# Kernel optimization log

Hardware: AMD Instinct MI355X
Metric: run time of the kernel (lower is better)

Reference implementation:

```python
import jax, jax.numpy as jnp
import numpy as np


def _conv(x, w, b):
    # x: [N,Cin,H,W], w: [Cout,Cin,kh,kw]
    y = jax.lax.conv_general_dilated(x, w, (1, 1), 'SAME',
                                     dimension_numbers=('NCHW', 'OIHW', 'NCHW'))
    return y + b[None, :, None, None]


def _up2(x):
    n, c, h, w = x.shape
    return jax.image.resize(x, (n, c, 2 * h, 2 * w), method='bilinear')


def setup_inputs() -> dict:
    key = jax.random.key(0)
    ks = jax.random.split(key, 24)
    N, C, H, W = 4, 256, 128, 128
    D, L, NUM_CLASSES = 512, 8, 75
    f32 = jnp.float32

    def rn(k, shape, scale=0.02):
        return jax.random.normal(k, shape, dtype=f32) * scale

    inp = {
        'p2': jax.random.normal(ks[0], (N, C, H, W), dtype=f32),
        'p3': jax.random.normal(ks[1], (N, C, H // 2, W // 2), dtype=f32),
        'p4': jax.random.normal(ks[2], (N, C, H // 4, W // 4), dtype=f32),
        'p5': jax.random.normal(ks[3], (N, C, H // 8, W // 8), dtype=f32),
        'rel_coord': jax.random.normal(ks[4], (N, 2, H, W), dtype=f32),
        'abs_coord': jax.random.normal(ks[5], (N, 2, H, W), dtype=f32),
        'fg_mask': jax.random.randint(ks[6], (N, 1, H, W), 0, 2, dtype=jnp.int32),
    }
    # scale-head convs: p2 x1 (no up), p3 x1 (+up), p4 x2 (+up each), p5 x3 (+up each)
    for i, nm in enumerate(['w_p2_0', 'w_p3_0', 'w_p4_0', 'w_p4_1', 'w_p5_0', 'w_p5_1', 'w_p5_2']):
        inp[nm] = rn(ks[7 + i], (C, C, 3, 3))
        inp['b' + nm[1:]] = jnp.zeros((C,), f32)
    # comb_pe_conv: (conv_dims + pe_dim) -> conv_dims, 3x3
    inp['comb_w'] = rn(ks[14], (C, C + 4, 3, 3))
    inp['comb_b'] = jnp.zeros((C,), f32)
    # densepose sparse head: 8 stacked submanifold 3x3 convs, dim 512
    inp['head_w0'] = rn(ks[15], (D, C, 3, 3))
    inp['head_b0'] = jnp.zeros((D,), f32)
    inp['head_w'] = rn(ks[16], (L - 1, D, D, 3, 3))
    inp['head_b'] = jnp.zeros((L - 1, D), f32)
    # predictor: 1x1 conv to num_classes
    inp['pred_w'] = rn(ks[17], (NUM_CLASSES, D, 1, 1))
    inp['pred_b'] = jnp.zeros((NUM_CLASSES,), f32)
    return inp


def reference(p2, p3, p4, p5, rel_coord, abs_coord, fg_mask,
              w_p2_0, b_p2_0, w_p3_0, b_p3_0, w_p4_0, b_p4_0, w_p4_1, b_p4_1,
              w_p5_0, b_p5_0, w_p5_1, b_p5_1, w_p5_2, b_p5_2,
              comb_w, comb_b, head_w0, head_b0, head_w, head_b, pred_w, pred_b):
    relu = jax.nn.relu
    # FPN scale heads merged to common stride
    x = relu(_conv(p2, w_p2_0, b_p2_0))
    x = x + _up2(relu(_conv(p3, w_p3_0, b_p3_0)))
    t = _up2(relu(_conv(p4, w_p4_0, b_p4_0)))
    x = x + _up2(relu(_conv(t, w_p4_1, b_p4_1)))
    t = _up2(relu(_conv(p5, w_p5_0, b_p5_0)))
    t = _up2(relu(_conv(t, w_p5_1, b_p5_1)))
    x = x + _up2(relu(_conv(t, w_p5_2, b_p5_2)))
    # concat positional encodings, comb conv
    x = jnp.concatenate([x, rel_coord, abs_coord], axis=1)  # [N, C+4, H, W]
    x = relu(_conv(x, comb_w, comb_b))
    # sparse gather -> submanifold sparse conv head -> dense scatter.
    # Masking inputs and outputs at each layer is math-equivalent to spconv's
    # SparseConvTensor built from fg_mask-active coords, SubM convs, then .dense().
    mask = (fg_mask > 0).astype(x.dtype)  # [N,1,H,W]
    h = x * mask
    h = relu(_conv(h, head_w0, head_b0)) * mask
    for i in range(head_w.shape[0]):
        h = relu(_conv(h, head_w[i], head_b[i])) * mask
    # dense predictor (1x1 conv) on scattered dense tensor
    return _conv(h, pred_w, pred_b)  # [N, 75, H, W]
```

## Files before the change

kernel.cpp:

```cpp
#include <hip/hip_runtime.h>
#include <cstdint>
#include <cstddef>

#define THREADS 256

typedef _Float16 f16x8 __attribute__((ext_vector_type(8)));
typedef _Float16 f16x4 __attribute__((ext_vector_type(4)));
typedef _Float16 f16x2 __attribute__((ext_vector_type(2)));
typedef float f32x4 __attribute__((ext_vector_type(4)));
typedef float f32x8 __attribute__((ext_vector_type(8)));

__device__ __forceinline__ void gll16(const void* g, void* l) {
    __builtin_amdgcn_global_load_lds(
        (const __attribute__((address_space(1))) unsigned int*)g,
        (__attribute__((address_space(3))) unsigned int*)l, 16, 0, 0);
}

__global__ void pack_scale_all_kernel(
    const float* __restrict__ w0, const float* __restrict__ w1,
    const float* __restrict__ w2, const float* __restrict__ w3,
    const float* __restrict__ w4, const float* __restrict__ w5,
    const float* __restrict__ w6, const float* __restrict__ w7,
    _Float16* __restrict__ wp)
{
    const int wi = blockIdx.y;
    const float* w = (wi == 0) ? w0 : (wi == 1) ? w1 : (wi == 2) ? w2 : (wi == 3) ? w3
                   : (wi == 4) ? w4 : (wi == 5) ? w5 : (wi == 6) ? w6 : w7;
    const int Cin = (wi == 7) ? 260 : 256;
    const int CC  = (wi == 7) ? 9 : 8;
    _Float16* dst = wp + (size_t)wi * 663552;
    int idx = blockIdx.x * THREADS + threadIdx.x;
    int total = 256 * CC * 4;
    if (idx >= total) return;
    int u = idx & 3;
    int cc = (idx >> 2) % CC;
    int co = (idx >> 2) / CC;
    int ci0 = cc * 32 + u * 8;
    for (int tap = 0; tap < 9; ++tap) {
        f16x8 v;
#pragma unroll
        for (int j = 0; j < 8; ++j) {
            int ci = ci0 + j;
            v[j] = (ci < Cin) ? (_Float16)w[((size_t)co * Cin + ci) * 9 + tap] : (_Float16)0.f;
        }
        *reinterpret_cast<f16x8*>(dst + ((((size_t)tap * CC + cc) * 4 + u) * 256 + co) * 8) = v;
    }
}

__global__ void pack_wdense_kernel(const float* __restrict__ w, _Float16* __restrict__ wp,
                                   int CinTrue, int CINP)
{
    const int NSTEP = 9 * (CINP / 64);
    int idx = blockIdx.x * THREADS + threadIdx.x;
    if (idx >= 256 * NSTEP * 8) return;
    int kc = idx & 7;
    int t = (idx >> 3) % NSTEP;
    int co = (idx >> 3) / NSTEP;
    int kcs = kc ^ (co & 7);
    int k = t * 64 + kcs * 8;
    int tap = k / CINP;
    int cib = k - tap * CINP;
    f16x8 v;
#pragma unroll
    for (int j = 0; j < 8; ++j) {
        int ci = cib + j;
        v[j] = (ci < CinTrue) ? (_Float16)w[((size_t)co * CinTrue + ci) * 9 + tap] : (_Float16)0.f;
    }
    *reinterpret_cast<f16x8*>(wp + ((size_t)t * 2048 + co * 8 + kc) * 8) = v;
}

__global__ void pack_whead_all_kernel(const float* __restrict__ hw0,
                                      const float* __restrict__ hw,
                                      _Float16* __restrict__ wp0,
                                      _Float16* __restrict__ wpH)
{
    const int wi = blockIdx.y;
    const int Cin = (wi == 0) ? 256 : 512;
    const float* w = (wi == 0) ? hw0 : hw + (size_t)(wi - 1) * 2359296;
    _Float16* wp = (wi == 0) ? wp0 : wpH + (size_t)(wi - 1) * 2359296;
    const int NSTEP = 9 * (Cin / 64);
    int idx = blockIdx.x * THREADS + threadIdx.x;
    int total = 512 * NSTEP * 8;
    if (idx >= total) return;
    int kc = idx & 7;
    int t = (idx >> 3) % NSTEP;
    int co = (idx >> 3) / NSTEP;
    int gy = co >> 8;
    int r = co & 255;
    int kcs = kc ^ (r & 7);
    int k = t * 64 + kcs * 8;
    int tap = k / Cin;
    int cib = k - tap * Cin;
    f16x8 v;
#pragma unroll
    for (int j = 0; j < 8; ++j)
        v[j] = (_Float16)w[((size_t)co * Cin + cib + j) * 9 + tap];
    *reinterpret_cast<f16x8*>(wp + ((size_t)(t * 2 + gy) * 2048 + r * 8 + kc) * 8) = v;
}

__global__ void zerows_kernel(float* __restrict__ p)
{
    p[blockIdx.x * THREADS + threadIdx.x] = 0.f;
}

__global__ void zero2_kernel(_Float16* __restrict__ a, _Float16* __restrict__ b)
{
    const size_t N = 4ull * 16384 * 512;
    for (size_t i = ((size_t)blockIdx.x * THREADS + threadIdx.x) * 8; i < N;
         i += (size_t)gridDim.x * THREADS * 8) {
        *reinterpret_cast<f16x8*>(a + i) = (f16x8){};
        *reinterpret_cast<f16x8*>(b + i) = (f16x8){};
    }
}

__global__ __launch_bounds__(1024)
void compact_kernel(const int* __restrict__ fg, int* __restrict__ list)
{
    __shared__ int part[1024];
    const int tid = threadIdx.x;
    const int base = tid * 64;
    int cnt = 0;
    for (int j = 0; j < 64; ++j) cnt += (fg[base + j] > 0) ? 1 : 0;
    part[tid] = cnt;
    __syncthreads();
    for (int off = 1; off < 1024; off <<= 1) {
        int v = (tid >= off) ? part[tid - off] : 0;
        __syncthreads();
        part[tid] += v;
        __syncthreads();
    }
    int pos = part[tid] - cnt;
    for (int j = 0; j < 64; ++j)
        if (fg[base + j] > 0) list[pos++] = base + j;
    const int total = part[1023];
    for (int i = total + tid; i < 40960; i += 1024) list[i] = -1;
}

__global__ __launch_bounds__(256)
void t_all_kernel(const float* __restrict__ s2, const float* __restrict__ s3,
                  const float* __restrict__ s4, const float* __restrict__ s5,
                  _Float16* __restrict__ d2, _Float16* __restrict__ d3,
                  _Float16* __restrict__ d4, _Float16* __restrict__ d5)
{
    __shared__ _Float16 tile[64 * 32];
    const int lvl = blockIdx.z >> 2;
    const int n = blockIdx.z & 3;
    const int HW = 16384 >> (2 * lvl);
    const int p0 = blockIdx.x * 64;
    if (p0 >= HW) return;
    const float* in = (lvl == 0) ? s2 : (lvl == 1) ? s3 : (lvl == 2) ? s4 : s5;
    _Float16* out = (lvl == 0) ? d2 : (lvl == 1) ? d3 : (lvl == 2) ? d4 : d5;
    const int C = 256;
    const int c0 = blockIdx.y * 32;
    const int tid = threadIdx.x;
    {
        int ci = tid >> 3;
        int j8 = (tid & 7) * 8;
        f32x8 v = *reinterpret_cast<const f32x8*>(in + ((size_t)n * C + c0 + ci) * HW + p0 + j8);
#pragma unroll
        for (int j = 0; j < 8; ++j)
            tile[(j8 + j) * 32 + ci] = (_Float16)v[j];
    }
    __syncthreads();
    {
        int px = tid >> 2;
        int u = tid & 3;
        f16x8 v = *reinterpret_cast<const f16x8*>(&tile[px * 32 + u * 8]);
        *reinterpret_cast<f16x8*>(out + ((size_t)n * HW + p0 + px) * C + c0 + u * 8) = v;
    }
}

template<int INF32, int OUTMODE, int CC>
__global__ __launch_bounds__(512, 4)
void convu_kernel(const void* __restrict__ inv, const _Float16* __restrict__ wp,
                  const float* __restrict__ bias, const int* __restrict__ msk,
                  void* __restrict__ outp, int Cout, int H, int W,
                  int inCst, int outCst, int useMask)
{
    __shared__ _Float16 Xs[2 * 1344 * 8];

    const int tid = threadIdx.x;
    const int lane = tid & 63;
    const int wave = tid >> 6;
    const int lm = lane & 15;
    const int lu = lane >> 4;
    const int waveco = (wave & 1) * 64;
    const int wrow = (wave >> 1) * 4;
    const int n = blockIdx.z;
    const int co0 = blockIdx.y * 128;
    const int tpr = W >> 4;
    const int tx = blockIdx.x % tpr;
    const int ty = blockIdx.x / tpr;
    const int x0 = tx << 4;
    const int y0 = ty << 4;
    const int HW = H * W;

    int soff[3];
#pragma unroll
    for (int t = 0; t < 3; ++t) {
        int s = tid + t * 512;
        int item = s >> 2, u = s & 3;
        int row = item / 18, col = item - row * 18;
        int y = y0 + row - 1, x = x0 + col - 1;
        soff[t] = (s < 1296 && y >= 0 && y < H && x >= 0 && x < W)
                      ? ((n * HW + y * W + x) * inCst + u * 8) : -1;
    }

    f32x4 acc[4][4];
#pragma unroll
    for (int m = 0; m < 4; ++m)
#pragma unroll
        for (int nf = 0; nf < 4; ++nf)
            acc[m][nf] = (f32x4){0.f, 0.f, 0.f, 0.f};

    const size_t tstride = (size_t)CC * 4 * Cout * 8;

    {
        const _Float16* src = (const _Float16*)inv;
#pragma unroll
        for (int t = 0; t < 3; ++t) {
            int s = tid + t * 512;
            if (s < 1296 && soff[t] < 0) {
                *reinterpret_cast<f16x8*>(&Xs[s * 8]) = (f16x8){};
                *reinterpret_cast<f16x8*>(&Xs[(1344 + s) * 8]) = (f16x8){};
            }
        }
#pragma unroll
        for (int t = 0; t < 3; ++t) {
            int s = tid + t * 512;
            if (s < 1296 && soff[t] >= 0)
                gll16(src + soff[t], &Xs[(t * 512 + (tid & ~63)) * 8]);
        }
    }
    __syncthreads();

    int bsel = 0;
    for (int cc = 0; cc < CC; ++cc) {
        if (cc + 1 < CC) {
            const _Float16* src = (const _Float16*)inv;
#pragma unroll
            for (int t = 0; t < 3; ++t) {
                int s = tid + t * 512;
                if (s < 1296 && soff[t] >= 0)
                    gll16(src + soff[t] + (cc + 1) * 32,
                          &Xs[((bsel ^ 1) * 1344 + t * 512 + (tid & ~63)) * 8]);
            }
        }
        {
            const int xbase = bsel * 1344;
            const _Float16* wb = wp + (((size_t)cc * 4 + lu) * Cout + co0 + waveco + lm) * 8;
#pragma unroll
            for (int tap = 0; tap < 9; ++tap) {
                const int dy = tap / 3, dx = tap % 3;
                const _Float16* wt = wb + (size_t)tap * tstride;
                f16x8 a[4], b[4];
#pragma unroll
                for (int m = 0; m < 4; ++m)
                    a[m] = *reinterpret_cast<const f16x8*>(wt + m * 128);
#pragma unroll
                for (int nf = 0; nf < 4; ++nf) {
                    int slot = ((wrow + nf + dy) * 18 + lm + dx) * 4 + lu;
                    b[nf] = *reinterpret_cast<const f16x8*>(&Xs[(xbase + slot) * 8]);
                }
#pragma unroll
                for (int m = 0; m < 4; ++m)
#pragma unroll
                    for (int nf = 0; nf < 4; ++nf)
                        acc[m][nf] = __builtin_amdgcn_mfma_f32_16x16x32_f16(a[m], b[nf], acc[m][nf], 0, 0, 0);
            }
        }
        __syncthreads();
        bsel ^= 1;
    }

    const int xE = x0 + lm;
    const size_t nHW = (size_t)n * HW;
#pragma unroll
    for (int nf = 0; nf < 4; ++nf) {
        const int y = y0 + wrow + nf;
        float mv = 1.f;
        if (useMask) mv = (msk[nHW + y * W + xE] > 0) ? 1.f : 0.f;
        const size_t pixo = (nHW + (size_t)y * W + xE) * outCst;
#pragma unroll
        for (int m = 0; m < 4; ++m) {
            const int cb = co0 + waveco + m * 16 + lu * 4;
            const f32x4 bv = *reinterpret_cast<const f32x4*>(bias + cb);
            if (OUTMODE == 0) {
                f16x4 h;
#pragma unroll
                for (int r = 0; r < 4; ++r)
                    h[r] = (_Float16)(fmaxf(acc[m][nf][r] + bv[r], 0.f) * mv);
                *reinterpret_cast<f16x4*>((_Float16*)outp + pixo + cb) = h;
            } else if (OUTMODE == 1) {
                f32x4 v;
#pragma unroll
                for (int r = 0; r < 4; ++r)
                    v[r] = fmaxf(acc[m][nf][r] + bv[r], 0.f);
                *reinterpret_cast<f32x4*>((float*)outp + pixo + cb) = v;
            } else {
                f32x4 old = *reinterpret_cast<const f32x4*>((float*)outp + pixo + cb);
#pragma unroll
                for (int r = 0; r < 4; ++r)
                    old[r] += fmaxf(acc[m][nf][r] + bv[r], 0.f);
                *reinterpret_cast<f32x4*>((float*)outp + pixo + cb) = old;
            }
        }
    }
}

template<int CINP, int MASK>
__global__ __launch_bounds__(512, 1)
void gemm_dense_kernel(const _Float16* __restrict__ in,
                       const _Float16* __restrict__ wpk,
                       const float* __restrict__ bias,
                       const int* __restrict__ fg,
                       _Float16* __restrict__ outp, int outCst,
                       const _Float16* __restrict__ zpage)
{
    constexpr int SPT = CINP / 64;
    __shared__ __attribute__((aligned(16))) char ldsb[2 * 65536];

    const int job = blockIdx.x;
    const int xcd = job & 7;
    const int idx = job >> 3;
    const int img = idx >> 3;
    const int tile = xcd * 8 + (idx & 7);
    const int x0 = (tile & 7) << 4;
    const int y0 = (tile >> 3) << 4;

    const int tid = threadIdx.x;
    const int lane = tid & 63;
    const int wave = tid >> 6;
    const int lm = lane & 15;
    const int lu = lane >> 4;
    const int wco = (wave & 1) * 128;
    const int wpx = (wave >> 1) * 64;

    const _Float16* bsrc = in + (size_t)img * 16384 * CINP;

    const _Float16* bptr[4];
    unsigned long long inbm = 0;
    int dstA[4], dstB[4];
#pragma unroll
    for (int s = 0; s < 4; ++s) {
        const int row = s * 64 + (tid >> 3);
        const int kc = (tid & 7) ^ (row & 7);
        const int y = y0 + (row >> 4);
        const int x = x0 + (row & 15);
        bptr[s] = bsrc + (size_t)(y * 128 + x) * CINP + kc * 8;
#pragma unroll
        for (int tap = 0; tap < 9; ++tap) {
            const int yy = y + tap / 3 - 1;
            const int xx = x + tap % 3 - 1;
            if ((unsigned)yy < 128u && (unsigned)xx < 128u)
                inbm |= 1ull << (s * 9 + tap);
        }
        dstA[s] = (s * 512 + (tid & ~63)) * 16;
        dstB[s] = 32768 + (s * 512 + (tid & ~63)) * 16;
    }

    auto STAGE = [&](int t, int bufByte) {
        const _Float16* as = wpk + (size_t)t * 16384;
#pragma unroll
        for (int s = 0; s < 4; ++s)
            gll16(as + (size_t)(s * 512 + tid) * 8, ldsb + bufByte + dstA[s]);
        const int tap = t / SPT;
        const int ci0 = (t % SPT) * 64;
        const int delta = ((tap / 3 - 1) * 128 + (tap % 3 - 1)) * CINP + ci0;
#pragma unroll
        for (int s = 0; s < 4; ++s) {
            const bool ok = (inbm >> (s * 9 + tap)) & 1ull;
            const _Float16* src = ok ? (bptr[s] + delta) : zpage;
            gll16(src, ldsb + bufByte + dstB[s]);
        }
    };

    f32x4 acc[8][4];
#pragma unroll
    for (int m = 0; m < 8; ++m)
#pragma unroll
        for (int n = 0; n < 4; ++n)
            acc[m][n] = (f32x4){0.f, 0.f, 0.f, 0.f};

    STAGE(0, 0);
    __syncthreads();

    int bsel = 0;
    for (int cb = 0; cb < SPT; ++cb) {
        for (int tap = 0; tap < 9; ++tap) {
            if (tap < 8) STAGE((tap + 1) * SPT + cb, (bsel ^ 1) * 65536);
            else if (cb + 1 < SPT) STAGE(cb + 1, (bsel ^ 1) * 65536);
            const int ab = bsel * 65536;
#pragma unroll
            for (int s = 0; s < 2; ++s) {
                f16x8 bfr[4];
#pragma unroll
                for (int n = 0; n < 4; ++n) {
                    const int row = wpx + n * 16 + lm;
                    const int ch = (s * 4 + lu) ^ (row & 7);
                    bfr[n] = *reinterpret_cast<const f16x8*>(ldsb + ab + 32768 + row * 128 + ch * 16);
                }
#pragma unroll
                for (int m = 0; m < 8; ++m) {
                    const int row = wco + m * 16 + lm;
                    const int ch = (s * 4 + lu) ^ (row & 7);
                    const f16x8 afr = *reinterpret_cast<const f16x8*>(ldsb + ab + row * 128 + ch * 16);
#pragma unroll
                    for (int n = 0; n < 4; ++n)
                        acc[m][n] = __builtin_amdgcn_mfma_f32_16x16x32_f16(afr, bfr[n], acc[m][n], 0, 0, 0);
                }
            }
            __syncthreads();
            bsel ^= 1;
        }
    }

    const int base = img * 16384;
#pragma unroll
    for (int n = 0; n < 4; ++n) {
        const int px = wpx + n * 16 + lm;
        const int y = y0 + (px >> 4), x = x0 + (px & 15);
        float mv = 1.f;
        if (MASK) mv = (fg[base + y * 128 + x] > 0) ? 1.f : 0.f;
        _Float16* pp = outp + ((size_t)base + y * 128 + x) * outCst + wco;
#pragma unroll
        for (int m = 0; m < 8; ++m) {
            const f32x4 bv = *reinterpret_cast<const f32x4*>(bias + wco + m * 16 + lu * 4);
            f16x4 h;
#pragma unroll
            for (int rr = 0; rr < 4; ++rr)
                h[rr] = (_Float16)(fmaxf(acc[m][n][rr] + bv[rr], 0.f) * mv);
            *reinterpret_cast<f16x4*>(pp + m * 16 + lu * 4) = h;
        }
    }
}

template<int CIN>
__global__ __launch_bounds__(512, 1)
void gemm_head_kernel(const _Float16* __restrict__ in,
                      const _Float16* __restrict__ wpk,
                      const float* __restrict__ bias,
                      const int* __restrict__ list,
                      _Float16* __restrict__ outp,
                      const _Float16* __restrict__ zpage)
{
    constexpr int SPT = CIN / 64;
    __shared__ __attribute__((aligned(16))) char ldsb[2 * 73728];

    const int job = blockIdx.x;
    const int xcd = job & 7;
    const int r8 = job >> 3;
    const int tile = xcd * 16 + (r8 >> 1);
    const int gy = r8 & 1;
    if (list[tile * 320] < 0) return;

    const int tid = threadIdx.x;
    const int lane = tid & 63;
    const int wave = tid >> 6;
    const int lm = lane & 15;
    const int lu = lane >> 4;
    const int wco = (wave & 1) * 128;
    const int g80 = (wave >> 1) * 80;
    const int co0 = gy * 256;

    const _Float16* bptr[5];
    unsigned long long inbm = 0;
    int dstA[4], dstB[5];
#pragma unroll
    for (int s = 0; s < 5; ++s) {
        const int row = s * 64 + (tid >> 3);
        const int kc = (tid & 7) ^ (row & 7);
        const int entry = list[tile * 320 + row];
        bptr[s] = zpage;
        if (entry >= 0) {
            const int y = (entry >> 7) & 127;
            const int x = entry & 127;
            bptr[s] = in + (size_t)entry * CIN + kc * 8;
#pragma unroll
            for (int tap = 0; tap < 9; ++tap) {
                const int yy = y + tap / 3 - 1;
                const int xx = x + tap % 3 - 1;
                if ((unsigned)yy < 128u && (unsigned)xx < 128u)
                    inbm |= 1ull << (s * 9 + tap);
            }
        }
        dstB[s] = 32768 + (s * 512 + (tid & ~63)) * 16;
    }
#pragma unroll
    for (int s = 0; s < 4; ++s) dstA[s] = (s * 512 + (tid & ~63)) * 16;

    auto STAGE = [&](int t, int bufByte) {
        const _Float16* as = wpk + (size_t)(t * 2 + gy) * 16384;
#pragma unroll
        for (int s = 0; s < 4; ++s)
            gll16(as + (size_t)(s * 512 + tid) * 8, ldsb + bufByte + dstA[s]);
        const int tap = t / SPT;
        const int ci0 = (t % SPT) * 64;
        const int delta = ((tap / 3 - 1) * 128 + (tap % 3 - 1)) * CIN + ci0;
#pragma unroll
        for (int s = 0; s < 5; ++s) {
            const bool ok = (inbm >> (s * 9 + tap)) & 1ull;
            const _Float16* src = ok ? (bptr[s] + delta) : zpage;
            gll16(src, ldsb + bufByte + dstB[s]);
        }
    };

    f32x4 acc[8][5];
#pragma unroll
    for (int m = 0; m < 8; ++m)
#pragma unroll
        for (int n = 0; n < 5; ++n)
            acc[m][n] = (f32x4){0.f, 0.f, 0.f, 0.f};

    STAGE(0, 0);
    __syncthreads();

    int bsel = 0;
    for (int cb = 0; cb < SPT; ++cb) {
        for (int tap = 0; tap < 9; ++tap) {
            if (tap < 8) STAGE((tap + 1) * SPT + cb, (bsel ^ 1) * 73728);
            else if (cb + 1 < SPT) STAGE(cb + 1, (bsel ^ 1) * 73728);
            const int ab = bsel * 73728;
#pragma unroll
            for (int s = 0; s < 2; ++s) {
                f16x8 bfr[5];
#pragma unroll
                for (int n = 0; n < 5; ++n) {
                    const int row = g80 + n * 16 + lm;
                    const int ch = (s * 4 + lu) ^ (row & 7);
                    bfr[n] = *reinterpret_cast<const f16x8*>(ldsb + ab + 32768 + row * 128 + ch * 16);
                }
#pragma unroll
                for (int m = 0; m < 8; ++m) {
                    const int row = wco + m * 16 + lm;
                    const int ch = (s * 4 + lu) ^ (row & 7);
                    const f16x8 afr = *reinterpret_cast<const f16x8*>(ldsb + ab + row * 128 + ch * 16);
#pragma unroll
                    for (int n = 0; n < 5; ++n)
                        acc[m][n] = __builtin_amdgcn_mfma_f32_16x16x32_f16(afr, bfr[n], acc[m][n], 0, 0, 0);
                }
            }
            __syncthreads();
            bsel ^= 1;
        }
    }

#pragma unroll
    for (int n = 0; n < 5; ++n) {
        const int entry = list[tile * 320 + g80 + n * 16 + lm];
        if (entry < 0) continue;
        _Float16* pp = outp + (size_t)entry * 512 + co0 + wco;
#pragma unroll
        for (int m = 0; m < 8; ++m) {
            const f32x4 bv = *reinterpret_cast<const f32x4*>(bias + co0 + wco + m * 16 + lu * 4);
            f16x4 h;
#pragma unroll
            for (int rr = 0; rr < 4; ++rr)
                h[rr] = (_Float16)fmaxf(acc[m][n][rr] + bv[rr], 0.f);
            *reinterpret_cast<f16x4*>(pp + m * 16 + lu * 4) = h;
        }
    }
}

__global__ void up2h_kernel(const _Float16* __restrict__ in, _Float16* __restrict__ out,
                            int Hin, int Win)
{
    const int Wout = Win << 1, Hout = Hin << 1;
    const int lw = __ffs(Wout) - 1, lh = __ffs(Hout) - 1;
    int i = blockIdx.x * THREADS + threadIdx.x;
    if (i >= 4 * Hout * Wout * 32) return;
    int u = i & 31;
    int p = i >> 5;
    int x = p & (Wout - 1);
    int y = (p >> lw) & (Hout - 1);
    int n = p >> (lw + lh);
    int iy = y >> 1, ix = x >> 1;
    int y2 = (y & 1) ? min(iy + 1, Hin - 1) : max(iy - 1, 0);
    int x2 = (x & 1) ? min(ix + 1, Win - 1) : max(ix - 1, 0);
    const _Float16* base = in + ((size_t)n * Hin * Win) * 256 + u * 8;
    f16x8 v00 = *reinterpret_cast<const f16x8*>(base + (iy * Win + ix) * 256);
    f16x8 v01 = *reinterpret_cast<const f16x8*>(base + (iy * Win + x2) * 256);
    f16x8 v10 = *reinterpret_cast<const f16x8*>(base + (y2 * Win + ix) * 256);
    f16x8 v11 = *reinterpret_cast<const f16x8*>(base + (y2 * Win + x2) * 256);
    f16x8 o;
#pragma unroll
    for (int j = 0; j < 8; ++j) {
        float v = 0.5625f * (float)v00[j] + 0.1875f * ((float)v01[j] + (float)v10[j])
                + 0.0625f * (float)v11[j];
        o[j] = (_Float16)v;
    }
    *reinterpret_cast<f16x8*>(out + (((size_t)n * Hout * Wout) + y * Wout + x) * 256 + u * 8) = o;
}

__global__ void up2addh_kernel(const float* __restrict__ in, _Float16* __restrict__ Xch)
{
    int i = blockIdx.x * THREADS + threadIdx.x;
    if (i >= 4 * 16384 * 32) return;
    int u = i & 31;
    int p = i >> 5;
    int x = p & 127;
    int y = (p >> 7) & 127;
    int n = p >> 14;
    int iy = y >> 1, ix = x >> 1;
    int y2 = (y & 1) ? min(iy + 1, 63) : max(iy - 1, 0);
    int x2 = (x & 1) ? min(ix + 1, 63) : max(ix - 1, 0);
    const float* base = in + ((size_t)n * 4096) * 256 + u * 8;
    f32x8 v00 = *reinterpret_cast<const f32x8*>(base + (iy * 64 + ix) * 256);
    f32x8 v01 = *reinterpret_cast<const f32x8*>(base + (iy * 64 + x2) * 256);
    f32x8 v10 = *reinterpret_cast<const f32x8*>(base + (y2 * 64 + ix) * 256);
    f32x8 v11 = *reinterpret_cast<const f32x8*>(base + (y2 * 64 + x2) * 256);
    _Float16* dst = Xch + ((size_t)n * 16384 + y * 128 + x) * 320 + u * 8;
    f16x8 d = *reinterpret_cast<const f16x8*>(dst);
#pragma unroll
    for (int j = 0; j < 8; ++j)
        d[j] = (_Float16)((float)d[j] + 0.5625f * v00[j]
               + 0.1875f * (v01[j] + v10[j]) + 0.0625f * v11[j]);
    *reinterpret_cast<f16x8*>(dst) = d;
}

__global__ void coords2h_kernel(const float* __restrict__ rel, const float* __restrict__ abs_,
                                _Float16* __restrict__ Xch)
{
    int i = blockIdx.x * THREADS + threadIdx.x;
    if (i >= 4 * 16384) return;
    int px = i & 16383;
    int n = i >> 14;
    _Float16* dst = Xch + ((size_t)n * 16384 + px) * 320 + 256;
    f16x8 v0 = (f16x8){};
    v0[0] = (_Float16)rel[((size_t)n * 2 + 0) * 16384 + px];
    v0[1] = (_Float16)rel[((size_t)n * 2 + 1) * 16384 + px];
    v0[2] = (_Float16)abs_[((size_t)n * 2 + 0) * 16384 + px];
    v0[3] = (_Float16)abs_[((size_t)n * 2 + 1) * 16384 + px];
    *reinterpret_cast<f16x8*>(dst) = v0;
#pragma unroll
    for (int b = 1; b < 8; ++b)
        *reinterpret_cast<f16x8*>(dst + b * 8) = (f16x8){};
}

__global__ __launch_bounds__(256)
void predh_kernel(const _Float16* __restrict__ in, const float* __restrict__ w,
                  const float* __restrict__ bias, float* __restrict__ out)
{
    __shared__ _Float16 lw[25 * 512];
    const int co0 = blockIdx.y * 25;
    const int n = blockIdx.z;
    for (int idx = threadIdx.x; idx < 25 * 512; idx += 256)
        lw[idx] = (_Float16)w[(size_t)(co0 + idx / 512) * 512 + (idx & 511)];
    __syncthreads();
    int px = blockIdx.x * 256 + threadIdx.x;
    const _Float16* ip = in + ((size_t)n * 16384 + px) * 512;
    float acc[25];
#pragma unroll
    for (int j = 0; j < 25; ++j) acc[j] = bias[co0 + j];
    for (int g = 0; g < 64; ++g) {
        union { f16x8 v; f16x2 p[4]; } xv;
        xv.v = *reinterpret_cast<const f16x8*>(ip + g * 8);
#pragma unroll
        for (int j = 0; j < 25; ++j) {
            union { f16x8 v; f16x2 p[4]; } wv;
            wv.v = *reinterpret_cast<const f16x8*>(&lw[j * 512 + g * 8]);
#if __has_builtin(__builtin_amdgcn_fdot2)
#pragma unroll
            for (int k = 0; k < 4; ++k)
                acc[j] = __builtin_amdgcn_fdot2(xv.p[k], wv.p[k], acc[j], false);
#else
#pragma unroll
            for (int k = 0; k < 8; ++k)
                acc[j] = fmaf((float)xv.v[k], (float)wv.v[k], acc[j]);
#endif
        }
    }
    float* op = out + ((size_t)n * 75) * 16384 + px;
#pragma unroll
    for (int j = 0; j < 25; ++j)
        op[(size_t)(co0 + j) * 16384] = acc[j];
}

extern "C" void kernel_launch(void* const* d_in, const int* in_sizes, int n_in,
                              void* d_out, int out_size, void* d_ws, size_t ws_size,
                              hipStream_t stream)
{
    const float* p2   = (const float*)d_in[0];
    const float* p3   = (const float*)d_in[1];
    const float* p4   = (const float*)d_in[2];
    const float* p5   = (const float*)d_in[3];
    const float* rel  = (const float*)d_in[4];
    const float* abs_ = (const float*)d_in[5];
    const int*   fg   = (const int*)d_in[6];
    const float* w_p2_0 = (const float*)d_in[7];
    const float* b_p2_0 = (const float*)d_in[8];
    const float* w_p3_0 = (const float*)d_in[9];
    const float* b_p3_0 = (const float*)d_in[10];
    const float* w_p4_0 = (const float*)d_in[11];
    const float* b_p4_0 = (const float*)d_in[12];
    const float* w_p4_1 = (const float*)d_in[13];
    const float* b_p4_1 = (const float*)d_in[14];
    const float* w_p5_0 = (const float*)d_in[15];
    const float* b_p5_0 = (const float*)d_in[16];
    const float* w_p5_1 = (const float*)d_in[17];
    const float* b_p5_1 = (const float*)d_in[18];
    const float* w_p5_2 = (const float*)d_in[19];
    const float* b_p5_2 = (const float*)d_in[20];
    const float* comb_w = (const float*)d_in[21];
    const float* comb_b = (const float*)d_in[22];
    const float* head_w0 = (const float*)d_in[23];
    const float* head_b0 = (const float*)d_in[24];
    const float* head_w  = (const float*)d_in[25];
    const float* head_b  = (const float*)d_in[26];
    const float* pred_w  = (const float*)d_in[27];
    const float* pred_b  = (const float*)d_in[28];

    float* ws = (float*)d_ws;
    _Float16* Xch     = (_Float16*)ws;
    _Float16* pingA   = (_Float16*)ws;
    _Float16* pingB   = (_Float16*)(ws + 18874368);
    float*    regD    = ws + 35651584;
    _Float16* p2h     = (_Float16*)regD;
    _Float16* combOut = (_Float16*)regD;
    float*    t64sum  = regD;
    _Float16* t64b    = (_Float16*)(regD + 4194304);
    _Float16* t64c    = (_Float16*)(regD + 5242880);
    _Float16* t32a    = (_Float16*)(regD + 6291456);
    _Float16* t32b    = (_Float16*)(regD + 6553600);
    _Float16* t32c    = (_Float16*)(regD + 6815744);
    _Float16* t16a    = (_Float16*)(regD + 7077888);
    _Float16* p3h     = (_Float16*)(ws + 44040192);
    _Float16* p4h     = (_Float16*)(ws + 46137344);
    _Float16* p5h     = (_Float16*)(ws + 46661632);
    _Float16* wpScale = (_Float16*)(ws + 46792704);
    float*    zpage   = ws + 49446912;
    _Float16* wpH0    = (_Float16*)(ws + 49447936);
    _Float16* wpH     = (_Float16*)(ws + 50037760);
    int*      actList = (int*)(ws + 58295296);
    _Float16* wpComb  = (_Float16*)(ws + 58336256);
    _Float16* wpDp2   = wpScale;

    auto wpS = [&](int i) { return wpScale + (size_t)i * 663552; };

    auto convu = [&](const void* in, const _Float16* wpk, const float* bs, void* outp,
                     int mode, int Cout, int H, int W,
                     int inCst, int outCst) {
        dim3 grid((W / 16) * (H / 16), Cout / 128, 4);
        dim3 blk(512);
        if (mode == 0)
            convu_kernel<0, 0, 8><<<grid, blk, 0, stream>>>(in, wpk, bs, fg, outp, Cout, H, W, inCst, outCst, 0);
        else if (mode == 1)
            convu_kernel<0, 1, 8><<<grid, blk, 0, stream>>>(in, wpk, bs, fg, outp, Cout, H, W, inCst, outCst, 0);
        else
            convu_kernel<0, 2, 8><<<grid, blk, 0, stream>>>(in, wpk, bs, fg, outp, Cout, H, W, inCst, outCst, 0);
    };
    auto up2h = [&](const _Float16* in, _Float16* out, int Hin, int Win) {
        int total = 4 * (Hin * 2) * (Win * 2) * 32;
        up2h_kernel<<<dim3((total + THREADS - 1) / THREADS), dim3(THREADS), 0, stream>>>(
            in, out, Hin, Win);
    };

    zerows_kernel<<<dim3(4), dim3(THREADS), 0, stream>>>(zpage);
    compact_kernel<<<dim3(1), dim3(1024), 0, stream>>>(fg, actList);
    pack_scale_all_kernel<<<dim3(36, 8), dim3(THREADS), 0, stream>>>(
        w_p2_0, w_p3_0, w_p4_0, w_p4_1, w_p5_0, w_p5_1, w_p5_2, comb_w, wpScale);
    pack_wdense_kernel<<<dim3(288), dim3(THREADS), 0, stream>>>(w_p2_0, wpDp2, 256, 256);
    pack_wdense_kernel<<<dim3(360), dim3(THREADS), 0, stream>>>(comb_w, wpComb, 260, 320);
    pack_whead_all_kernel<<<dim3(1152, 8), dim3(THREADS), 0, stream>>>(
        head_w0, head_w, wpH0, wpH);
    t_all_kernel<<<dim3(256, 8, 16), dim3(256), 0, stream>>>(
        p2, p3, p4, p5, p2h, p3h, p4h, p5h);

    gemm_dense_kernel<256, 0><<<dim3(256), dim3(512), 0, stream>>>(
        p2h, wpDp2, b_p2_0, fg, Xch, 320, (const _Float16*)zpage);
    coords2h_kernel<<<dim3(256), dim3(THREADS), 0, stream>>>(rel, abs_, Xch);

    convu(p3h, wpS(1), b_p3_0, t64sum, 1, 256, 64, 64, 256, 256);

    convu(p4h, wpS(2), b_p4_0, t32a, 0, 256, 32, 32, 256, 256);
    up2h(t32a, t64b, 32, 32);
    convu(t64b, wpS(3), b_p4_1, t64sum, 2, 256, 64, 64, 256, 256);

    convu(p5h, wpS(4), b_p5_0, t16a, 0, 256, 16, 16, 256, 256);
    up2h(t16a, t32b, 16, 16);
    convu(t32b, wpS(5), b_p5_1, t32c, 0, 256, 32, 32, 256, 256);
    up2h(t32c, t64c, 32, 32);
    convu(t64c, wpS(6), b_p5_2, t64sum, 2, 256, 64, 64, 256, 256);

    up2addh_kernel<<<dim3(8192), dim3(THREADS), 0, stream>>>(t64sum, Xch);

    gemm_dense_kernel<320, 1><<<dim3(256), dim3(512), 0, stream>>>(
        Xch, wpComb, comb_b, fg, combOut, 256, (const _Float16*)zpage);

    zero2_kernel<<<dim3(4096), dim3(THREADS), 0, stream>>>(pingA, pingB);

    gemm_head_kernel<256><<<dim3(256), dim3(512), 0, stream>>>(
        combOut, wpH0, head_b0, actList, pingA, (const _Float16*)zpage);
    {
        const _Float16* s = pingA;
        _Float16* d = pingB;
        for (int i = 0; i < 7; ++i) {
            gemm_head_kernel<512><<<dim3(256), dim3(512), 0, stream>>>(
                s, wpH + (size_t)i * 2359296, head_b + (size_t)i * 512, actList, d,
                (const _Float16*)zpage);
            _Float16* tmp = (_Float16*)s; s = d; d = tmp;
        }
    }

    predh_kernel<<<dim3(64, 3, 4), dim3(256), 0, stream>>>(pingB, pred_w, pred_b, (float*)d_out);
}
```

Baseline: 2.212 ms.

## Shrink head GEMM tiles and drop double buffering to raise occupancy

The sparse head conv GEMM tile goes from 256 output channels by 320 pixels to 128 channels by 256 pixels, and the grid grows from 256 to 640 blocks. The weight packing changes to match the 4-way channel split. The double-buffered LDS pipeline is replaced with a single 48KB buffer, and the launch bounds now ask for 4 blocks per CU, so several blocks can overlap each other's loads. In exchange the kernel loses explicit load/compute overlap and adds a sync per step. It also tightens the register budget, which risks spills and more reloads of weights and activations across channel groups.

```diff
diff --git a/kernel.cpp b/kernel.cpp
--- a/kernel.cpp
+++ b/kernel.cpp
@@ -85,8 +85,8 @@
     int kc = idx & 7;
     int t = (idx >> 3) % NSTEP;
     int co = (idx >> 3) / NSTEP;
-    int gy = co >> 8;
-    int r = co & 255;
+    int gy = co >> 7;
+    int r = co & 127;
     int kcs = kc ^ (r & 7);
     int k = t * 64 + kcs * 8;
     int tap = k / Cin;
@@ -95,7 +95,7 @@
 #pragma unroll
     for (int j = 0; j < 8; ++j)
         v[j] = (_Float16)w[((size_t)co * Cin + cib + j) * 9 + tap];
-    *reinterpret_cast<f16x8*>(wp + ((size_t)(t * 2 + gy) * 2048 + r * 8 + kc) * 8) = v;
+    *reinterpret_cast<f16x8*>(wp + ((size_t)(t * 4 + gy) * 1024 + r * 8 + kc) * 8) = v;
 }
 
 __global__ void zerows_kernel(float* __restrict__ p)
@@ -436,7 +436,7 @@
 }
 
 template<int CIN>
-__global__ __launch_bounds__(512, 1)
+__global__ __launch_bounds__(512, 4)
 void gemm_head_kernel(const _Float16* __restrict__ in,
                       const _Float16* __restrict__ wpk,
                       const float* __restrict__ bias,
@@ -445,32 +445,31 @@
                       const _Float16* __restrict__ zpage)
 {
     constexpr int SPT = CIN / 64;
-    __shared__ __attribute__((aligned(16))) char ldsb[2 * 73728];
+    __shared__ __attribute__((aligned(16))) char ldsb[49152];
 
     const int job = blockIdx.x;
     const int xcd = job & 7;
     const int r8 = job >> 3;
-    const int tile = xcd * 16 + (r8 >> 1);
-    const int gy = r8 & 1;
-    if (list[tile * 320] < 0) return;
+    const int tile = xcd * 20 + (r8 >> 2);
+    const int gy = r8 & 3;
+    if (list[tile * 256] < 0) return;
 
     const int tid = threadIdx.x;
     const int lane = tid & 63;
     const int wave = tid >> 6;
     const int lm = lane & 15;
     const int lu = lane >> 4;
-    const int wco = (wave & 1) * 128;
-    const int g80 = (wave >> 1) * 80;
-    const int co0 = gy * 256;
-
-    const _Float16* bptr[5];
+    const int wco = (wave & 1) * 64;
+    const int g64 = (wave >> 1) * 64;
+    const int co0 = gy * 128;
+
+    const _Float16* bptr[4];
     unsigned long long inbm = 0;
-    int dstA[4], dstB[5];
-#pragma unroll
-    for (int s = 0; s < 5; ++s) {
+#pragma unroll
+    for (int s = 0; s < 4; ++s) {
         const int row = s * 64 + (tid >> 3);
         const int kc = (tid & 7) ^ (row & 7);
-        const int entry = list[tile * 320 + row];
+        const int entry = list[tile * 256 + row];
         bptr[s] = zpage;
         if (entry >= 0) {
             const int y = (entry >> 7) & 127;
@@ -484,74 +483,65 @@
                     inbm |= 1ull << (s * 9 + tap);
             }
         }
-        dstB[s] = 32768 + (s * 512 + (tid & ~63)) * 16;
-    }
-#pragma unroll
-    for (int s = 0; s < 4; ++s) dstA[s] = (s * 512 + (tid & ~63)) * 16;
-
-    auto STAGE = [&](int t, int bufByte) {
-        const _Float16* as = wpk + (size_t)(t * 2 + gy) * 16384;
-#pragma unroll
-        for (int s = 0; s < 4; ++s)
-            gll16(as + (size_t)(s * 512 + tid) * 8, ldsb + bufByte + dstA[s]);
+    }
+    const int ldst = (tid & ~63) * 16;
+
+    auto STAGE = [&](int t) {
+        const _Float16* as = wpk + (size_t)(t * 4 + gy) * 8192;
+        gll16(as + (size_t)tid * 8, ldsb + ldst);
+        gll16(as + (size_t)(512 + tid) * 8, ldsb + 8192 + ldst);
         const int tap = t / SPT;
         const int ci0 = (t % SPT) * 64;
         const int delta = ((tap / 3 - 1) * 128 + (tap % 3 - 1)) * CIN + ci0;
 #pragma unroll
-        for (int s = 0; s < 5; ++s) {
+        for (int s = 0; s < 4; ++s) {
             const bool ok = (inbm >> (s * 9 + tap)) & 1ull;
             const _Float16* src = ok ? (bptr[s] + delta) : zpage;
-            gll16(src, ldsb + bufByte + dstB[s]);
+            gll16(src, ldsb + 16384 + s * 8192 + ldst);
         }
     };
 
-    f32x4 acc[8][5];
-#pragma unroll
-    for (int m = 0; m < 8; ++m)
-#pragma unroll
-        for (int n = 0; n < 5; ++n)
+    f32x4 acc[4][4];
+#pragma unroll
+    for (int m = 0; m < 4; ++m)
+#pragma unroll
+        for (int n = 0; n < 4; ++n)
             acc[m][n] = (f32x4){0.f, 0.f, 0.f, 0.f};
 
-    STAGE(0, 0);
-    __syncthreads();
-
-    int bsel = 0;
     for (int cb = 0; cb < SPT; ++cb) {
         for (int tap = 0; tap < 9; ++tap) {
-            if (tap < 8) STAGE((tap + 1) * SPT + cb, (bsel ^ 1) * 73728);
-            else if (cb + 1 < SPT) STAGE(cb + 1, (bsel ^ 1) * 73728);
-            const int ab = bsel * 73728;
+            STAGE(tap * SPT + cb);
+            __syncthreads();
 #pragma unroll
             for (int s = 0; s < 2; ++s) {
-                f16x8 bfr[5];
-#pragma unroll
-                for (int n = 0; n < 5; ++n) {
-                    const int row = g80 + n * 16 + lm;
+                f16x8 bfr[4];
+#pragma unroll
+                for (int n = 0; n < 4; ++n) {
+                    const int row = g64 + n * 16 + lm;
                     const int ch = (s * 4 + lu) ^ (row & 7);
-                    bfr[n] = *reinterpret_cast<const f16x8*>(ldsb + ab + 32768 + row * 128 + ch * 16);
+                    bfr[n] = *reinterpret_cast<const f16x8*>(ldsb + 16384 + row * 128 + ch * 16);
                 }
 #pragma unroll
-                for (int m = 0; m < 8; ++m) {
+                for (int m = 0; m < 4; ++m) {
                     const int row = wco + m * 16 + lm;
                     const int ch = (s * 4 + lu) ^ (row & 7);
-                    const f16x8 afr = *reinterpret_cast<const f16x8*>(ldsb + ab + row * 128 + ch * 16);
-#pragma unroll
-                    for (int n = 0; n < 5; ++n)
+                    const f16x8 afr = *reinterpret_cast<const f16x8*>(ldsb + row * 128 + ch * 16);
+#pragma unroll
+                    for (int n = 0; n < 4; ++n)
                         acc[m][n] = __builtin_amdgcn_mfma_f32_16x16x32_f16(afr, bfr[n], acc[m][n], 0, 0, 0);
                 }
             }
             __syncthreads();
-            bsel ^= 1;
-        }
-    }
-
-#pragma unroll
-    for (int n = 0; n < 5; ++n) {
-        const int entry = list[tile * 320 + g80 + n * 16 + lm];
+        }
+    }
+
+#pragma unroll
+    for (int n = 0; n < 4; ++n) {
+        const int entry = list[tile * 256 + g64 + n * 16 + lm];
         if (entry < 0) continue;
         _Float16* pp = outp + (size_t)entry * 512 + co0 + wco;
 #pragma unroll
-        for (int m = 0; m < 8; ++m) {
+        for (int m = 0; m < 4; ++m) {
             const f32x4 bv = *reinterpret_cast<const f32x4*>(bias + co0 + wco + m * 16 + lu * 4);
             f16x4 h;
 #pragma unroll
@@ -789,13 +779,13 @@
 
     zero2_kernel<<<dim3(4096), dim3(THREADS), 0, stream>>>(pingA, pingB);
 
-    gemm_head_kernel<256><<<dim3(256), dim3(512), 0, stream>>>(
+    gemm_head_kernel<256><<<dim3(640), dim3(512), 0, stream>>>(
         combOut, wpH0, head_b0, actList, pingA, (const _Float16*)zpage);
     {
         const _Float16* s = pingA;
         _Float16* d = pingB;
         for (int i = 0; i < 7; ++i) {
-            gemm_head_kernel<512><<<dim3(256), dim3(512), 0, stream>>>(
+            gemm_head_kernel<512><<<dim3(640), dim3(512), 0, stream>>>(
                 s, wpH + (size_t)i * 2359296, head_b + (size_t)i * 512, actList, d,
                 (const _Float16*)zpage);
             _Float16* tmp = (_Float16*)s; s = d; d = tmp;
```

Measured after the change: 3.037 ms. +37.3%, slower.
